# Performance work log

Measured on AMD Instinct MI355X. Metric: run time of the kernel, lower is better.

Reference implementation:

```python
import jax, jax.numpy as jnp
import numpy as np
import math

D_MODEL = 1024
N_HEADS = 16
HEAD_DIM = D_MODEL // N_HEADS
PAD_INDEX = 0
NEG_INF = -1e9  # matches torch masked_fill value


def setup_inputs() -> dict:
    key = jax.random.key(0)
    ks = jax.random.split(key, 10)
    b, s = 2, 2048
    x = jax.random.normal(ks[0], (b, s, D_MODEL), dtype=jnp.float32)
    input_ids = jax.random.randint(ks[1], (b, s), 0, 32000, dtype=jnp.int64)
    scale = 1.0 / math.sqrt(D_MODEL)
    def lin(k):
        kw, kb = jax.random.split(k)
        W = jax.random.uniform(kw, (D_MODEL, D_MODEL), jnp.float32, -scale, scale)
        bb = jax.random.uniform(kb, (D_MODEL,), jnp.float32, -scale, scale)
        return W, bb
    Wq, bq = lin(ks[2])
    Wk, bk = lin(ks[3])
    Wv, bv = lin(ks[4])
    Wo, bo = lin(ks[5])
    return {"x": x, "input_ids": input_ids,
            "Wq": Wq, "bq": bq, "Wk": Wk, "bk": bk,
            "Wv": Wv, "bv": bv, "Wo": Wo, "bo": bo}


def reference(x, input_ids, Wq, bq, Wk, bk, Wv, bv, Wo, bo):
    b, s, _ = x.shape
    # torch nn.Linear: y = x @ W.T + b
    q = (x @ Wq.T + bq).reshape(b, s, N_HEADS, HEAD_DIM)
    k = (x @ Wk.T + bk).reshape(b, s, N_HEADS, HEAD_DIM)
    v = (x @ Wv.T + bv).reshape(b, s, N_HEADS, HEAD_DIM)
    # scores: [b, h, s, s]
    scores = jnp.einsum('bqhd,bkhd->bhqk', q, k) / math.sqrt(HEAD_DIM)
    pad_mask = (input_ids != PAD_INDEX)[:, None, None, :]          # [b,1,1,s] over keys
    causal = jnp.tril(jnp.ones((s, s), dtype=bool))[None, None]     # [1,1,s,s]
    final_mask = pad_mask & causal
    scores = jnp.where(final_mask, scores, NEG_INF)
    attn = jax.nn.softmax(scores, axis=-1)
    out = jnp.einsum('bhqk,bkhd->bqhd', attn, v).reshape(b, s, D_MODEL)
    return out @ Wo.T + bo
```

## Files before the change

### kernel.cpp

```cpp
#include <hip/hip_runtime.h>

#define DMODEL 1024
#define NHEADS 16
#define HDIM   64
#define BATCH  2
#define SEQ    2048
#define MROWS  (BATCH*SEQ)

typedef __bf16 bf16x8 __attribute__((ext_vector_type(8)));
typedef __bf16 bf16x4 __attribute__((ext_vector_type(4)));
typedef float floatx4 __attribute__((ext_vector_type(4)));

typedef const __attribute__((address_space(1))) void gvoid;
typedef __attribute__((address_space(3))) void lvoid;

#define QSCALE 0.18033688011112042f

__global__ void cast_all(const float* __restrict__ x,
                         const float* __restrict__ wq, const float* __restrict__ wk,
                         const float* __restrict__ wv, const float* __restrict__ wo,
                         __bf16* __restrict__ xb, __bf16* __restrict__ wqb,
                         __bf16* __restrict__ wkb, __bf16* __restrict__ wvb,
                         __bf16* __restrict__ wob)
{
  const int i = blockIdx.x * 256 + threadIdx.x;
  const float* s; __bf16* o; int off;
  if (i < MROWS*DMODEL/4) { s = x; o = xb; off = i; }
  else {
    const int r = i - MROWS*DMODEL/4;
    const int w = r >> 18;
    off = r & 262143;
    s = (w == 0) ? wq : (w == 1) ? wk : (w == 2) ? wv : wo;
    o = (w == 0) ? wqb : (w == 1) ? wkb : (w == 2) ? wvb : wob;
  }
  const float4 f = ((const float4*)s)[off];
  bf16x4 v = {(__bf16)f.x, (__bf16)f.y, (__bf16)f.z, (__bf16)f.w};
  *(bf16x4*)(o + off*4) = v;
}

template<int MODE>
__global__ __launch_bounds__(256, 3)
void gemm_nt(const unsigned short* __restrict__ A,
             const unsigned short* __restrict__ W0,
             const unsigned short* __restrict__ W1,
             const unsigned short* __restrict__ W2,
             const float* __restrict__ b0,
             const float* __restrict__ b1,
             const float* __restrict__ b2,
             unsigned short* __restrict__ qout,
             unsigned short* __restrict__ kout,
             unsigned short* __restrict__ vout,
             float* __restrict__ outf)
{
  const int K = DMODEL;
  __shared__ unsigned short As[2][128*32];
  __shared__ unsigned short Bs[2][128*32];
  const int tid  = threadIdx.x;
  const int wid  = tid >> 6;
  const int lane = tid & 63;

  const int lin = blockIdx.x;
  const int wg  = (MODE == 0) ? ((lin & 7)*96 + (lin >> 3))
                              : ((lin & 7)*32 + (lin >> 3));
  const int bx  = (MODE == 0) ? (wg % 24) : (wg & 7);
  const int by  = (MODE == 0) ? (wg / 24) : (wg >> 3);
  const int brow = by * 128;
  const int bcol = bx * 128;
  const int wr = (wid >> 1) * 64;
  const int wc = (wid & 1) * 64;

  int which = 0;
  const unsigned short* Bw = W0;
  const float* bias = b0;
  int bcolL = bcol;
  if (MODE == 0) {
    which = bcol >> 10;
    Bw   = which == 0 ? W0 : which == 1 ? W1 : W2;
    bias = which == 0 ? b0 : which == 1 ? b1 : b2;
    bcolL = bcol & 1023;
  }

  floatx4 acc[4][4] = {};

  const int sr = wid*16 + (lane >> 2);
  const int sc = (lane & 3) * 8;
  const int fr = lane & 15;
  const int fk = (lane >> 4) * 8;

#define GSTAGE(KT, B) do {                                                     \
    _Pragma("unroll")                                                          \
    for (int i_ = 0; i_ < 2; ++i_) {                                           \
      __builtin_amdgcn_global_load_lds(                                        \
          (gvoid*)(A + (size_t)(brow + i_*64 + sr)*K + (KT) + sc),             \
          (lvoid*)(As[B] + i_*2048 + wid*512), 16, 0, 0);                      \
      __builtin_amdgcn_global_load_lds(                                        \
          (gvoid*)(Bw + (size_t)(bcolL + i_*64 + sr)*K + (KT) + sc),           \
          (lvoid*)(Bs[B] + i_*2048 + wid*512), 16, 0, 0);                      \
    }                                                                          \
  } while (0)

  GSTAGE(0, 0);

  for (int kt = 0; kt < K; kt += 32) {
    const int cur = (kt >> 5) & 1;
    if (kt + 32 < K) {
      GSTAGE(kt + 32, cur ^ 1);
      asm volatile("s_waitcnt vmcnt(4)" ::: "memory");
    } else {
      asm volatile("s_waitcnt vmcnt(0)" ::: "memory");
    }
    __builtin_amdgcn_s_barrier();
    __builtin_amdgcn_sched_barrier(0);

    bf16x8 af[4], bfv[4];
#pragma unroll
    for (int m = 0; m < 4; ++m)
      af[m] = *(const bf16x8*)(As[cur] + (wr + m*16 + fr)*32 + fk);
#pragma unroll
    for (int n = 0; n < 4; ++n)
      bfv[n] = *(const bf16x8*)(Bs[cur] + (wc + n*16 + fr)*32 + fk);
    __builtin_amdgcn_s_setprio(1);
#pragma unroll
    for (int m = 0; m < 4; ++m)
#pragma unroll
      for (int n = 0; n < 4; ++n)
        acc[m][n] = __builtin_amdgcn_mfma_f32_16x16x32_bf16(af[m], bfv[n], acc[m][n], 0, 0, 0);
    __builtin_amdgcn_s_setprio(0);
    __builtin_amdgcn_s_barrier();
  }
#undef GSTAGE

  const int er = (lane >> 4) * 4;
  const int ec = lane & 15;
#pragma unroll
  for (int m = 0; m < 4; ++m) {
#pragma unroll
    for (int n = 0; n < 4; ++n) {
      const int colL = bcolL + wc + n*16 + ec;
      const float bv = bias[colL];
      const int rowb = brow + wr + m*16 + er;
      if (MODE == 0) {
        const int bi = rowb >> 11, s = rowb & 2047;
        const int hh = colL >> 6, dd = colL & 63;
        if (which == 2) {
          bf16x4 v4 = {(__bf16)(acc[m][n][0] + bv), (__bf16)(acc[m][n][1] + bv),
                       (__bf16)(acc[m][n][2] + bv), (__bf16)(acc[m][n][3] + bv)};
          *(bf16x4*)((__bf16*)vout + ((size_t)(bi*NHEADS + hh)*HDIM + dd)*SEQ + s) = v4;
        } else if (which == 0) {
          __bf16* o = (__bf16*)qout;
#pragma unroll
          for (int j = 0; j < 4; ++j)
            o[((size_t)(bi*NHEADS + hh)*SEQ + s + j)*HDIM + dd] =
                (__bf16)((acc[m][n][j] + bv) * QSCALE);
        } else {
          __bf16* o = (__bf16*)kout;
#pragma unroll
          for (int j = 0; j < 4; ++j)
            o[((size_t)(bi*NHEADS + hh)*SEQ + s + j)*HDIM + dd] = (__bf16)(acc[m][n][j] + bv);
        }
      } else {
#pragma unroll
        for (int j = 0; j < 4; ++j)
          outf[(size_t)(rowb + j)*DMODEL + colL] = acc[m][n][j] + bv;
      }
    }
  }
}

__global__ __launch_bounds__(512, 4)
void attn_fwd(const unsigned short* __restrict__ qb,
              const unsigned short* __restrict__ kb,
              const unsigned short* __restrict__ vtb,
              const int* __restrict__ ids,
              unsigned short* __restrict__ outb)
{
  const int hb = blockIdx.x;
  const int h = hb & 15, bi = hb >> 4;
  const int y = blockIdx.y;
  const int jm = y >> 3, mm = y & 7;
  const int qt = jm*8 + ((jm & 1) ? 7 - mm : mm);

  const int tid = threadIdx.x, wid = tid >> 6, lane = tid & 63;
  const int grp  = wid >> 2;
  const int wid4 = wid & 3;
  const int qbase = qt * 64;
  const size_t hoff = (size_t)(bi*NHEADS + h) * SEQ * HDIM;
  const unsigned short* Qh  = qb  + hoff;
  const unsigned short* Kh  = kb  + hoff;
  const unsigned short* Vth = vtb + hoff;

  __shared__ unsigned short Ks[2][64*64];
  __shared__ unsigned short Vs[2][64*64];
  float* LOf = (float*)Vs;
  float* Ll  = (float*)Ks;

  const int q_   = lane & 15;
  const int hi4  = lane >> 4;
  const int koff = hi4 * 4;
  const int qg = qbase + wid4*16 + q_;

  bf16x8 qf[2];
#pragma unroll
  for (int c = 0; c < 2; ++c)
    qf[c] = *(const bf16x8*)(Qh + (size_t)qg*HDIM + c*32 + hi4*8);

  const int gt = tid & 255;
  const int r0 = gt >> 3;
  const int sw = ((gt & 7) ^ (r0 & 7)) * 8;
  unsigned short* Pw = Ks[grp] + wid4*1024;

#define STAGE(T) do {                                                          \
    const unsigned short* kbase_ = Kh + (size_t)((T)*64) * HDIM;               \
    const unsigned short* vbase_ = Vth + (T)*64;                               \
    __builtin_amdgcn_global_load_lds((gvoid*)(kbase_ + r0*64 + sw),            \
                                     (lvoid*)(Ks[grp] + gt*8), 16, 0, 0);      \
    __builtin_amdgcn_global_load_lds((gvoid*)(kbase_ + (r0+32)*64 + sw),       \
                                     (lvoid*)(Ks[grp] + (gt+256)*8), 16, 0, 0);\
    __builtin_amdgcn_global_load_lds((gvoid*)(vbase_ + (size_t)r0*SEQ + sw),   \
                                     (lvoid*)(Vs[grp] + gt*8), 16, 0, 0);      \
    __builtin_amdgcn_global_load_lds((gvoid*)(vbase_ + (size_t)(r0+32)*SEQ + sw),\
                                     (lvoid*)(Vs[grp] + (gt+256)*8), 16, 0, 0);\
  } while (0)

  float lsum = 0.f;
  floatx4 Oacc[4] = {};

  const int nT = qt + 1;
  const int h0 = (nT + 1) >> 1;
  const int cnt = (grp == 0) ? h0 : nT - h0;
  const int tb  = (grp == 0) ? 0 : h0;

  for (int i = 0; i < h0; ++i) {
    const bool valid = (i < cnt);
    const int t = tb + i;
    const int kb0 = t * 64;
    int pvv = 1;
    if (valid) {
      pvv = ids[bi*SEQ + kb0 + lane];
      STAGE(t);
    }
    asm volatile("s_waitcnt vmcnt(0)" ::: "memory");
    const unsigned long long wm = __ballot(pvv == 0);
    __builtin_amdgcn_s_barrier();
    __builtin_amdgcn_sched_barrier(0);

    floatx4 st[4];
    if (valid) {
#pragma unroll
      for (int t2 = 0; t2 < 4; ++t2) {
        st[t2] = (floatx4){0.f, 0.f, 0.f, 0.f};
        const int kr = t2*16 + q_;
#pragma unroll
        for (int c = 0; c < 2; ++c) {
          const int cd = ((c*4 + hi4) ^ (kr & 7)) * 8;
          bf16x8 kf = *(const bf16x8*)(Ks[grp] + kr*64 + cd);
          st[t2] = __builtin_amdgcn_mfma_f32_16x16x32_bf16(kf, qf[c], st[t2], 0, 0, 0);
        }
      }
    }
    __syncthreads();

    if (valid) {
      const bool maskstep = (t == nT - 1) || (wm != 0ull);
      float p[16];
      if (!maskstep) {
#pragma unroll
        for (int j = 0; j < 16; ++j) p[j] = exp2f(st[j >> 2][j & 3]);
      } else {
#pragma unroll
        for (int t2 = 0; t2 < 4; ++t2)
#pragma unroll
          for (int r = 0; r < 4; ++r) {
            const int ko = t2*16 + koff + r;
            const bool dead = ((kb0 + ko) > qg) || (((wm >> ko) & 1ull) != 0ull);
            p[t2*4+r] = dead ? 0.f : exp2f(st[t2][r]);
          }
      }
      float ps = 0.f;
#pragma unroll
      for (int t2 = 0; t2 < 4; ++t2) {
        ps += ((p[t2*4] + p[t2*4+1]) + (p[t2*4+2] + p[t2*4+3]));
        bf16x4 pk = {(__bf16)p[t2*4], (__bf16)p[t2*4+1], (__bf16)p[t2*4+2], (__bf16)p[t2*4+3]};
        const int ko = t2*16 + koff;
        *(bf16x4*)(Pw + q_*64 + (((ko >> 3) ^ (q_ & 7)) * 8) + (ko & 7)) = pk;
      }
      lsum += ps;

      __builtin_amdgcn_s_setprio(1);
#pragma unroll
      for (int cp = 0; cp < 2; ++cp) {
        const int ko = cp*32 + hi4*8;
        bf16x8 pf = *(const bf16x8*)(Pw + q_*64 + (((ko >> 3) ^ (q_ & 7)) * 8));
#pragma unroll
        for (int n = 0; n < 4; ++n) {
          const int d = n*16 + q_;
          const int cd = ((cp*4 + hi4) ^ (d & 7)) * 8;
          bf16x8 vf = *(const bf16x8*)(Vs[grp] + d*64 + cd);
          Oacc[n] = __builtin_amdgcn_mfma_f32_16x16x32_bf16(pf, vf, Oacc[n], 0, 0, 0);
        }
      }
      __builtin_amdgcn_s_setprio(0);
    }
    __syncthreads();
  }
#undef STAGE

  float lt = lsum + __shfl_xor(lsum, 16);
  lt += __shfl_xor(lt, 32);

  if (grp == 1) {
#pragma unroll
    for (int r = 0; r < 4; ++r)
#pragma unroll
      for (int n = 0; n < 4; ++n)
        LOf[(wid4*16 + koff + r)*64 + n*16 + q_] = Oacc[n][r];
    if (hi4 == 0) Ll[wid4*16 + q_] = lt;
  }
  __syncthreads();
  if (grp == 0) {
#pragma unroll
    for (int r = 0; r < 4; ++r) {
      const int rloc = wid4*16 + koff + r;
      const float inv = 1.f / (__shfl(lt, koff + r) + Ll[rloc]);
      const int row = bi*SEQ + qbase + rloc;
#pragma unroll
      for (int n = 0; n < 4; ++n) {
        const float o = Oacc[n][r] + LOf[rloc*64 + n*16 + q_];
        ((__bf16*)outb)[(size_t)row*DMODEL + h*HDIM + n*16 + q_] = (__bf16)(o * inv);
      }
    }
  }
}

extern "C" void kernel_launch(void* const* d_in, const int* in_sizes, int n_in,
                              void* d_out, int out_size, void* d_ws, size_t ws_size,
                              hipStream_t stream)
{
  const float* x  = (const float*)d_in[0];
  const int*   ids= (const int*)d_in[1];
  const float* Wq = (const float*)d_in[2];
  const float* bq = (const float*)d_in[3];
  const float* Wk = (const float*)d_in[4];
  const float* bk = (const float*)d_in[5];
  const float* Wv = (const float*)d_in[6];
  const float* bv = (const float*)d_in[7];
  const float* Wo = (const float*)d_in[8];
  const float* bo = (const float*)d_in[9];
  float* out = (float*)d_out;

  char* ws = (char*)d_ws;
  unsigned short* xb   = (unsigned short*)(ws);
  unsigned short* wqb  = (unsigned short*)(ws + ( 8u<<20));
  unsigned short* wkb  = (unsigned short*)(ws + (10u<<20));
  unsigned short* wvb  = (unsigned short*)(ws + (12u<<20));
  unsigned short* wob  = (unsigned short*)(ws + (14u<<20));
  unsigned short* qbuf = (unsigned short*)(ws + (16u<<20));
  unsigned short* kbuf = (unsigned short*)(ws + (24u<<20));
  unsigned short* vbuf = (unsigned short*)(ws + (32u<<20));
  unsigned short* abuf = (unsigned short*)(ws + (40u<<20));

  cast_all<<<8192, 256, 0, stream>>>(x, Wq, Wk, Wv, Wo,
                                     (__bf16*)xb, (__bf16*)wqb, (__bf16*)wkb,
                                     (__bf16*)wvb, (__bf16*)wob);

  gemm_nt<0><<<768, 256, 0, stream>>>(xb, wqb, wkb, wvb, bq, bk, bv,
                                      qbuf, kbuf, vbuf, nullptr);

  attn_fwd<<<dim3(32, 32), 512, 0, stream>>>(qbuf, kbuf, vbuf, ids, abuf);

  gemm_nt<1><<<256, 256, 0, stream>>>(abuf, wob, wob, wob, bo, bo, bo,
                                      nullptr, nullptr, nullptr, out);
}
```

Before: 119.2 us.

## Rewrite attention with 32x32 MFMA, register P path, and 4-way KV split

The attention kernel moves from 16x16x32 to 32x32x16 bf16 MFMA tiles. P is now packed to bf16 in registers and exchanged with permlane32_swap instead of a round trip through shared memory. The key range is split across four wave groups of two waves each rather than two groups of four, and the next tile is prefetched after the barrier. Blocks are launched heaviest-first with a 1D grid. This aims to cut LDS traffic and barriers and to balance causal work better, at the cost of more shared memory (two extra K/V buffers) and a four-way reduction at the end.

Measured after the change: 135.0 us. 13.2% more time.

```diff
diff --git a/kernel.cpp b/kernel.cpp
--- a/kernel.cpp
+++ b/kernel.cpp
@@ -10,11 +10,19 @@
 typedef __bf16 bf16x8 __attribute__((ext_vector_type(8)));
 typedef __bf16 bf16x4 __attribute__((ext_vector_type(4)));
 typedef float floatx4 __attribute__((ext_vector_type(4)));
+typedef float floatx16 __attribute__((ext_vector_type(16)));
+typedef unsigned int uintx2 __attribute__((ext_vector_type(2)));
 
 typedef const __attribute__((address_space(1))) void gvoid;
 typedef __attribute__((address_space(3))) void lvoid;
 
 #define QSCALE 0.18033688011112042f
+
+__device__ inline unsigned cvtpk(float lo, float hi) {
+  unsigned w;
+  asm("v_cvt_pk_bf16_f32 %0, %1, %2" : "=v"(w) : "v"(lo), "v"(hi));
+  return w;
+}
 
 __global__ void cast_all(const float* __restrict__ x,
                          const float* __restrict__ wq, const float* __restrict__ wk,
@@ -174,160 +182,164 @@
               const int* __restrict__ ids,
               unsigned short* __restrict__ outb)
 {
-  const int hb = blockIdx.x;
+  const int bx = blockIdx.x;
+  const int hb = bx & 31;
+  const int qt = 31 - (bx >> 5);
   const int h = hb & 15, bi = hb >> 4;
-  const int y = blockIdx.y;
-  const int jm = y >> 3, mm = y & 7;
-  const int qt = jm*8 + ((jm & 1) ? 7 - mm : mm);
 
   const int tid = threadIdx.x, wid = tid >> 6, lane = tid & 63;
-  const int grp  = wid >> 2;
-  const int wid4 = wid & 3;
+  const int grp  = wid >> 1;
+  const int wrow = wid & 1;
   const int qbase = qt * 64;
   const size_t hoff = (size_t)(bi*NHEADS + h) * SEQ * HDIM;
   const unsigned short* Qh  = qb  + hoff;
   const unsigned short* Kh  = kb  + hoff;
   const unsigned short* Vth = vtb + hoff;
 
-  __shared__ unsigned short Ks[2][64*64];
-  __shared__ unsigned short Vs[2][64*64];
-  float* LOf = (float*)Vs;
-  float* Ll  = (float*)Ks;
-
-  const int q_   = lane & 15;
-  const int hi4  = lane >> 4;
-  const int koff = hi4 * 4;
-  const int qg = qbase + wid4*16 + q_;
-
-  bf16x8 qf[2];
-#pragma unroll
-  for (int c = 0; c < 2; ++c)
-    qf[c] = *(const bf16x8*)(Qh + (size_t)qg*HDIM + c*32 + hi4*8);
-
-  const int gt = tid & 255;
-  const int r0 = gt >> 3;
-  const int sw = ((gt & 7) ^ (r0 & 7)) * 8;
-  unsigned short* Pw = Ks[grp] + wid4*1024;
+  __shared__ unsigned short Ks[4][64*64];
+  __shared__ unsigned short Vs[4][64*64];
+  __shared__ float Lbuf[4][64];
+
+  const int q_ = lane & 31;
+  const int hi = lane >> 5;
+  const int qg = qbase + wrow*32 + q_;
+
+  bf16x8 qf[4];
+#pragma unroll
+  for (int dc = 0; dc < 4; ++dc)
+    qf[dc] = *(const bf16x8*)(Qh + (size_t)qg*HDIM + dc*16 + hi*8);
+
+  const int gt = tid & 127;
+  const int grow = gt >> 3;
+  const int gsw  = ((gt & 7) ^ (grow & 7)) * 8;
+  __bf16* OB = (grp == 1) ? (__bf16*)Ks :
+               (grp == 2) ? (__bf16*)(Ks[2]) : (__bf16*)Vs;
 
 #define STAGE(T) do {                                                          \
     const unsigned short* kbase_ = Kh + (size_t)((T)*64) * HDIM;               \
     const unsigned short* vbase_ = Vth + (T)*64;                               \
-    __builtin_amdgcn_global_load_lds((gvoid*)(kbase_ + r0*64 + sw),            \
-                                     (lvoid*)(Ks[grp] + gt*8), 16, 0, 0);      \
-    __builtin_amdgcn_global_load_lds((gvoid*)(kbase_ + (r0+32)*64 + sw),       \
-                                     (lvoid*)(Ks[grp] + (gt+256)*8), 16, 0, 0);\
-    __builtin_amdgcn_global_load_lds((gvoid*)(vbase_ + (size_t)r0*SEQ + sw),   \
-                                     (lvoid*)(Vs[grp] + gt*8), 16, 0, 0);      \
-    __builtin_amdgcn_global_load_lds((gvoid*)(vbase_ + (size_t)(r0+32)*SEQ + sw),\
-                                     (lvoid*)(Vs[grp] + (gt+256)*8), 16, 0, 0);\
+    _Pragma("unroll")                                                          \
+    for (int i_ = 0; i_ < 4; ++i_) {                                           \
+      __builtin_amdgcn_global_load_lds(                                        \
+          (gvoid*)(kbase_ + (size_t)(i_*16 + grow)*HDIM + gsw),                \
+          (lvoid*)(Ks[grp] + (i_*128 + gt)*8), 16, 0, 0);                      \
+      __builtin_amdgcn_global_load_lds(                                        \
+          (gvoid*)(vbase_ + (size_t)(i_*16 + grow)*SEQ + gsw),                 \
+          (lvoid*)(Vs[grp] + (i_*128 + gt)*8), 16, 0, 0);                      \
+    }                                                                          \
   } while (0)
 
   float lsum = 0.f;
-  floatx4 Oacc[4] = {};
+  floatx16 Oacc[2] = {};
 
   const int nT = qt + 1;
-  const int h0 = (nT + 1) >> 1;
-  const int cnt = (grp == 0) ? h0 : nT - h0;
-  const int tb  = (grp == 0) ? 0 : h0;
-
-  for (int i = 0; i < h0; ++i) {
+  const int base = nT >> 2, rem = nT & 3;
+  const int cnt = base + (grp < rem);
+  const int tb  = grp*base + ((grp < rem) ? grp : rem);
+  const int Hi  = base + (rem ? 1 : 0);
+
+  if (cnt > 0) STAGE(tb);
+
+  for (int i = 0; i < Hi; ++i) {
     const bool valid = (i < cnt);
     const int t = tb + i;
     const int kb0 = t * 64;
     int pvv = 1;
-    if (valid) {
-      pvv = ids[bi*SEQ + kb0 + lane];
-      STAGE(t);
-    }
+    if (valid) pvv = ids[bi*SEQ + kb0 + lane];
     asm volatile("s_waitcnt vmcnt(0)" ::: "memory");
     const unsigned long long wm = __ballot(pvv == 0);
     __builtin_amdgcn_s_barrier();
     __builtin_amdgcn_sched_barrier(0);
 
-    floatx4 st[4];
-    if (valid) {
-#pragma unroll
-      for (int t2 = 0; t2 < 4; ++t2) {
-        st[t2] = (floatx4){0.f, 0.f, 0.f, 0.f};
-        const int kr = t2*16 + q_;
-#pragma unroll
-        for (int c = 0; c < 2; ++c) {
-          const int cd = ((c*4 + hi4) ^ (kr & 7)) * 8;
-          bf16x8 kf = *(const bf16x8*)(Ks[grp] + kr*64 + cd);
-          st[t2] = __builtin_amdgcn_mfma_f32_16x16x32_bf16(kf, qf[c], st[t2], 0, 0, 0);
-        }
-      }
-    }
-    __syncthreads();
-
     if (valid) {
       const bool maskstep = (t == nT - 1) || (wm != 0ull);
-      float p[16];
-      if (!maskstep) {
-#pragma unroll
-        for (int j = 0; j < 16; ++j) p[j] = exp2f(st[j >> 2][j & 3]);
-      } else {
-#pragma unroll
-        for (int t2 = 0; t2 < 4; ++t2)
-#pragma unroll
-          for (int r = 0; r < 4; ++r) {
-            const int ko = t2*16 + koff + r;
-            const bool dead = ((kb0 + ko) > qg) || (((wm >> ko) & 1ull) != 0ull);
-            p[t2*4+r] = dead ? 0.f : exp2f(st[t2][r]);
+#pragma unroll
+      for (int H = 0; H < 2; ++H) {
+        floatx16 st = {};
+        const int kr = H*32 + q_;
+        __builtin_amdgcn_s_setprio(1);
+#pragma unroll
+        for (int dc = 0; dc < 4; ++dc) {
+          const int ch = ((dc*2 + hi) ^ (q_ & 7)) * 8;
+          bf16x8 kf = *(const bf16x8*)(Ks[grp] + kr*64 + ch);
+          st = __builtin_amdgcn_mfma_f32_32x32x16_bf16(kf, qf[dc], st, 0, 0, 0);
+        }
+        __builtin_amdgcn_s_setprio(0);
+
+        float p[16];
+        float ps = 0.f;
+        if (!maskstep) {
+#pragma unroll
+          for (int r = 0; r < 16; ++r) { p[r] = exp2f(st[r]); ps += p[r]; }
+        } else {
+#pragma unroll
+          for (int r = 0; r < 16; ++r) {
+            const int crow = (r & 3) + 4*hi + 8*(r >> 2);
+            const int kglob = kb0 + H*32 + crow;
+            const bool dead = (kglob > qg) || (((wm >> (H*32 + crow)) & 1ull) != 0ull);
+            p[r] = dead ? 0.f : exp2f(st[r]);
+            ps += p[r];
           }
+        }
+        lsum += ps;
+
+        __builtin_amdgcn_s_setprio(1);
+#pragma unroll
+        for (int b = 0; b < 2; ++b) {
+          unsigned W0 = cvtpk(p[8*b+0], p[8*b+1]);
+          unsigned W1 = cvtpk(p[8*b+2], p[8*b+3]);
+          unsigned W2 = cvtpk(p[8*b+4], p[8*b+5]);
+          unsigned W3 = cvtpk(p[8*b+6], p[8*b+7]);
+          uintx2 s02 = __builtin_amdgcn_permlane32_swap(W0, W2, false, false);
+          uintx2 s13 = __builtin_amdgcn_permlane32_swap(W1, W3, false, false);
+          union { unsigned u[4]; bf16x8 v; } af;
+          af.u[0] = s02[0]; af.u[1] = s13[0]; af.u[2] = s02[1]; af.u[3] = s13[1];
+          const int s = H*2 + b;
+#pragma unroll
+          for (int n = 0; n < 2; ++n) {
+            const int d = n*32 + q_;
+            const int ch = ((s*2 + hi) ^ (d & 7)) * 8;
+            bf16x8 vf = *(const bf16x8*)(Vs[grp] + d*64 + ch);
+            Oacc[n] = __builtin_amdgcn_mfma_f32_32x32x16_bf16(af.v, vf, Oacc[n], 0, 0, 0);
+          }
+        }
+        __builtin_amdgcn_s_setprio(0);
       }
-      float ps = 0.f;
-#pragma unroll
-      for (int t2 = 0; t2 < 4; ++t2) {
-        ps += ((p[t2*4] + p[t2*4+1]) + (p[t2*4+2] + p[t2*4+3]));
-        bf16x4 pk = {(__bf16)p[t2*4], (__bf16)p[t2*4+1], (__bf16)p[t2*4+2], (__bf16)p[t2*4+3]};
-        const int ko = t2*16 + koff;
-        *(bf16x4*)(Pw + q_*64 + (((ko >> 3) ^ (q_ & 7)) * 8) + (ko & 7)) = pk;
-      }
-      lsum += ps;
-
-      __builtin_amdgcn_s_setprio(1);
-#pragma unroll
-      for (int cp = 0; cp < 2; ++cp) {
-        const int ko = cp*32 + hi4*8;
-        bf16x8 pf = *(const bf16x8*)(Pw + q_*64 + (((ko >> 3) ^ (q_ & 7)) * 8));
-#pragma unroll
-        for (int n = 0; n < 4; ++n) {
-          const int d = n*16 + q_;
-          const int cd = ((cp*4 + hi4) ^ (d & 7)) * 8;
-          bf16x8 vf = *(const bf16x8*)(Vs[grp] + d*64 + cd);
-          Oacc[n] = __builtin_amdgcn_mfma_f32_16x16x32_bf16(pf, vf, Oacc[n], 0, 0, 0);
-        }
-      }
-      __builtin_amdgcn_s_setprio(0);
-    }
-    __syncthreads();
+    }
+    __builtin_amdgcn_s_barrier();
+    if (i + 1 < cnt) STAGE(t + 1);
   }
 #undef STAGE
 
-  float lt = lsum + __shfl_xor(lsum, 16);
-  lt += __shfl_xor(lt, 32);
-
-  if (grp == 1) {
-#pragma unroll
-    for (int r = 0; r < 4; ++r)
-#pragma unroll
-      for (int n = 0; n < 4; ++n)
-        LOf[(wid4*16 + koff + r)*64 + n*16 + q_] = Oacc[n][r];
-    if (hi4 == 0) Ll[wid4*16 + q_] = lt;
-  }
+  float lt = lsum + __shfl_xor(lsum, 32);
+
+  float* B1 = (float*)Ks;
+  float* B2 = B1 + 4096;
+  float* B3 = (float*)Vs;
+  float* OBf = (grp == 1) ? B1 : (grp == 2) ? B2 : B3;
+  if (grp >= 1) {
+#pragma unroll
+    for (int r = 0; r < 16; ++r) {
+      const int row = wrow*32 + (r & 3) + 4*hi + 8*(r >> 2);
+      OBf[row*64 + q_]      = Oacc[0][r];
+      OBf[row*64 + 32 + q_] = Oacc[1][r];
+    }
+  }
+  if (hi == 0) Lbuf[grp][wrow*32 + q_] = lt;
   __syncthreads();
+
   if (grp == 0) {
 #pragma unroll
-    for (int r = 0; r < 4; ++r) {
-      const int rloc = wid4*16 + koff + r;
-      const float inv = 1.f / (__shfl(lt, koff + r) + Ll[rloc]);
-      const int row = bi*SEQ + qbase + rloc;
-#pragma unroll
-      for (int n = 0; n < 4; ++n) {
-        const float o = Oacc[n][r] + LOf[rloc*64 + n*16 + q_];
-        ((__bf16*)outb)[(size_t)row*DMODEL + h*HDIM + n*16 + q_] = (__bf16)(o * inv);
-      }
+    for (int r = 0; r < 16; ++r) {
+      const int row = wrow*32 + (r & 3) + 4*hi + 8*(r >> 2);
+      const int rq = row & 63;
+      const float den = Lbuf[0][rq] + Lbuf[1][rq] + Lbuf[2][rq] + Lbuf[3][rq];
+      const float inv = 1.f / den;
+      const float o0 = Oacc[0][r] + B1[row*64 + q_] + B2[row*64 + q_] + B3[row*64 + q_];
+      const float o1 = Oacc[1][r] + B1[row*64 + 32 + q_] + B2[row*64 + 32 + q_] + B3[row*64 + 32 + q_];
+      const size_t grow_ = (size_t)(bi*SEQ + qbase + row);
+      ((__bf16*)outb)[grow_*DMODEL + h*HDIM + q_]      = (__bf16)(o0 * inv);
+      ((__bf16*)outb)[grow_*DMODEL + h*HDIM + 32 + q_] = (__bf16)(o1 * inv);
     }
   }
 }
@@ -366,7 +378,7 @@
   gemm_nt<0><<<768, 256, 0, stream>>>(xb, wqb, wkb, wvb, bq, bk, bv,
                                       qbuf, kbuf, vbuf, nullptr);
 
-  attn_fwd<<<dim3(32, 32), 512, 0, stream>>>(qbuf, kbuf, vbuf, ids, abuf);
+  attn_fwd<<<1024, 512, 0, stream>>>(qbuf, kbuf, vbuf, ids, abuf);
 
   gemm_nt<1><<<256, 256, 0, stream>>>(abuf, wob, wob, wob, bo, bo, bo,
                                       nullptr, nullptr, nullptr, out);
```
